# Performance work log

Measured on AMD Instinct MI355X. Metric: run time of the kernel, lower is better.

The kernel has to match this reference:

```python
import jax, jax.numpy as jnp
import numpy as np

N, NC, E, S = 65536, 24576, 524288, 256
VAR_DIM, H1, H2, H3, H4 = 6, 128, 128, 256, 128
THRE, EPS = 0.7, 1e-5


def _bn(x, g, b):
    # BatchNorm1d, training-mode batch statistics (biased var), dropout treated as identity
    mu = x.mean(0)
    v = x.var(0)
    return (x - mu) * jax.lax.rsqrt(v + EPS) * g + b


def _gcn_sparse(h, src, dst, ew, W, b):
    # PyG GCNConv with edge weights: add self-loops (weight 1), symmetric normalization
    n = h.shape[0]
    loop = jnp.arange(n)
    s = jnp.concatenate([src, loop])
    d = jnp.concatenate([dst, loop])
    w = jnp.concatenate([ew, jnp.ones((n,), h.dtype)])
    deg = jax.ops.segment_sum(w, d, num_segments=n)
    dinv = jnp.where(deg > 0, jax.lax.rsqrt(deg), 0.0)
    norm = dinv[s] * w * dinv[d]
    xw = h @ W.T  # [n, out]
    out = jax.ops.segment_sum(norm[:, None] * xw[s], d, num_segments=n)
    return out + b


def _gcn_dense(h, A, W, b):
    # GCNConv on a dense binary adjacency (no edge weights), self-loops + sym norm
    n = h.shape[0]
    A_hat = A + jnp.eye(n, dtype=h.dtype)
    deg = A_hat.sum(0)
    dinv = jnp.where(deg > 0, jax.lax.rsqrt(deg), 0.0)
    return dinv[:, None] * (A_hat.T @ ((h @ W.T) * dinv[:, None])) + b


def setup_inputs() -> dict:
    key = jax.random.key(0)
    ks = jax.random.split(key, 10)

    def w(k, o, i):
        return jax.random.normal(k, (o, i), jnp.float32) / np.float32(np.sqrt(i))

    x = jax.random.normal(ks[0], (N, VAR_DIM), jnp.float32)
    edge_attr = jax.random.uniform(ks[1], (E,), jnp.float32)
    scen_adj = jax.random.uniform(ks[2], (S, S), jnp.float32)
    edge_index = jax.random.randint(ks[3], (2, E), 0, N)
    batch = jnp.arange(N) // (N // S)  # sorted node->graph ids, 256 nodes per graph
    mark = jnp.concatenate([jnp.ones((NC,), jnp.int32), jnp.zeros((N - NC,), jnp.int32)])
    return {
        "x": x, "edge_attr": edge_attr, "scen_adj": scen_adj,
        "mlp_var_w": w(ks[4], H1, VAR_DIM), "mlp_var_b": jnp.zeros((H1,), jnp.float32),
        "mlp_con_w": w(ks[5], H1, 1), "mlp_con_b": jnp.zeros((H1,), jnp.float32),
        "conv1_w": w(ks[6], H2, H1), "conv1_b": jnp.zeros((H2,), jnp.float32),
        "conv2_w": w(ks[7], H3, H2), "conv2_b": jnp.zeros((H3,), jnp.float32),
        "conv3_w": w(ks[8], H4, H3), "conv3_b": jnp.zeros((H4,), jnp.float32),
        "bn1_g": jnp.ones((H1,), jnp.float32), "bn1_b": jnp.zeros((H1,), jnp.float32),
        "bn2_g": jnp.ones((H2,), jnp.float32), "bn2_b": jnp.zeros((H2,), jnp.float32),
        "bn3_g": jnp.ones((H3,), jnp.float32), "bn3_b": jnp.zeros((H3,), jnp.float32),
        "mark": mark, "edge_index": edge_index, "batch": batch, "n_con": NC,
    }


def reference(x, edge_attr, scen_adj, mlp_var_w, mlp_var_b, mlp_con_w, mlp_con_b,
              conv1_w, conv1_b, conv2_w, conv2_b, conv3_w, conv3_b,
              bn1_g, bn1_b, bn2_g, bn2_b, bn3_g, bn3_b,
              mark, edge_index, batch, n_con):
    nc = int(n_con)  # mark layout: first nc nodes are constraints (mark==1), rest vars
    con_feat = jnp.tanh(x[:nc, 0:1] @ mlp_con_w.T + mlp_con_b)
    var_feat = jnp.tanh(x[nc:] @ mlp_var_w.T + mlp_var_b)
    h = jnp.concatenate([con_feat, var_feat], axis=0)  # [N, H1], con-first as in torch cat
    h = _bn(h, bn1_g, bn1_b)  # dropout = identity (eval)
    h = _gcn_sparse(h, edge_index[0], edge_index[1], edge_attr, conv1_w, conv1_b)
    h = jnp.tanh(_bn(h, bn2_g, bn2_b))
    s = scen_adj.shape[0]
    sums = jax.ops.segment_sum(h, batch, num_segments=s)
    cnt = jax.ops.segment_sum(jnp.ones((h.shape[0],), h.dtype), batch, num_segments=s)
    pooled = sums / jnp.maximum(cnt, 1.0)[:, None]  # global_mean_pool -> [S, H2]
    A = (scen_adj >= THRE).astype(h.dtype)  # filter_adj + unweighted edges
    f = jnp.tanh(_bn(_gcn_dense(pooled, A, conv2_w, conv2_b), bn3_g, bn3_b))
    feat = jnp.tanh(_gcn_dense(f, A, conv3_w, conv3_b))
    return feat, feat.mean(0)
```

## Files before the change

kernel.cpp:

```cpp
#include <hip/hip_runtime.h>
#include <hip/hip_bf16.h>
#include <cstddef>

#define N_NODES 65536
#define N_EDGES 524288
#define S_GRAPH 256
#define BN_EPS 1e-5f
#define THRE 0.7f

typedef __hip_bfloat16 bf16;
typedef unsigned int uint32;
typedef unsigned char uchar;
typedef unsigned short ushort16;
typedef __attribute__((ext_vector_type(8))) short short8;
typedef __attribute__((ext_vector_type(4))) float f32x4;

__device__ __forceinline__ float blo(uint32 u) { return __uint_as_float(u << 16); }
__device__ __forceinline__ float bhi(uint32 u) { return __uint_as_float(u & 0xffff0000u); }

__device__ __forceinline__ uint32 packbf(float a, float b)
{
    bf16 ha = __float2bfloat16(a), hb = __float2bfloat16(b);
    unsigned short ua, ub;
    __builtin_memcpy(&ua, &ha, 2); __builtin_memcpy(&ub, &hb, 2);
    return (uint32)ua | ((uint32)ub << 16);
}

__device__ __forceinline__ float ftanh(float x)
{
    float e = __builtin_amdgcn_exp2f(x * 2.8853900817779268f);
    return 1.0f - 2.0f * __builtin_amdgcn_rcpf(e + 1.0f);
}

__global__ __launch_bounds__(256) void k_mlp_hist(
    const float* __restrict__ x, const float* __restrict__ wv,
    const float* __restrict__ bv, const float* __restrict__ wc,
    const float* __restrict__ bc, const int* __restrict__ nconp,
    uint32* __restrict__ h0u, float* __restrict__ pstat,
    const int* __restrict__ dst, uint32* __restrict__ blkhist,
    const float* __restrict__ scen, float* __restrict__ fcol,
    const float* __restrict__ w1f, uint32* __restrict__ w1bk,
    float* __restrict__ zacc, int* __restrict__ ctrs)
{
    __shared__ float xs[128 * 6];
    __shared__ float sh[256];
    __shared__ uint32 bh[256];
    int t = threadIdx.x;
    int b = blockIdx.x;
    if (b < 512) {
        bh[t] = 0;
        __syncthreads();
        int e0 = b * 1024 + t * 4;
        int4 d4 = *(const int4*)(dst + e0);
        atomicAdd(&bh[d4.x >> 8], 1u);
        atomicAdd(&bh[d4.y >> 8], 1u);
        atomicAdd(&bh[d4.z >> 8], 1u);
        atomicAdd(&bh[d4.w >> 8], 1u);
        __syncthreads();
        blkhist[b * 256 + t] = bh[t];
        return;
    }
    if (b >= 1024) {
        if (b == 1024) {
            float s = 0.f;
            for (int r = 0; r < 256; r++)
                s += (scen[r * 256 + t] >= THRE) ? 1.0f : 0.0f;
            fcol[t] = s;
        } else if (b == 1056) {
            const float4* w4 = (const float4*)w1f;
            uint2* wo = (uint2*)w1bk;
            #pragma unroll
            for (int it = 0; it < 16; it++) {
                int fi = it * 256 + t;
                float4 w = w4[fi];
                wo[fi] = make_uint2(packbf(w.x, w.y), packbf(w.z, w.w));
            }
            for (int i = t; i < 7168; i += 256) zacc[i] = 0.f;
            if (t < 8) ctrs[t] = 0;
        }
        return;
    }
    int n0 = (b - 512) * 128;
    if (t < 192) ((float4*)xs)[t] = ((const float4*)(x + (size_t)n0 * 6))[t];
    __syncthreads();

    int nc = *nconp;
    int lane = t & 63, wave = t >> 6;
    int j0 = 2 * lane;
    const float2* wv2 = (const float2*)wv;
    float2 wa0 = wv2[j0 * 3], wa1 = wv2[j0 * 3 + 1], wa2 = wv2[j0 * 3 + 2];
    float2 wb0 = wv2[j0 * 3 + 3], wb1 = wv2[j0 * 3 + 4], wb2 = wv2[j0 * 3 + 5];
    float wc0 = wc[j0], wc1 = wc[j0 + 1], bc0 = bc[j0], bc1 = bc[j0 + 1];
    float bv0 = bv[j0], bv1 = bv[j0 + 1];

    float s0 = 0.f, ss0 = 0.f, s1 = 0.f, ss1 = 0.f;
    #pragma unroll 4
    for (int m = 0; m < 32; m++) {
        int ln = wave * 32 + m;
        int n = n0 + ln;
        const float* xr = &xs[ln * 6];
        float a0, a1;
        if (n < nc) {
            float xv = xr[0];
            a0 = xv * wc0 + bc0; a1 = xv * wc1 + bc1;
        } else {
            float x0 = xr[0], x1 = xr[1], x2 = xr[2], x3 = xr[3], x4 = xr[4], x5 = xr[5];
            a0 = bv0 + x0 * wa0.x + x1 * wa0.y + x2 * wa1.x + x3 * wa1.y + x4 * wa2.x + x5 * wa2.y;
            a1 = bv1 + x0 * wb0.x + x1 * wb0.y + x2 * wb1.x + x3 * wb1.y + x4 * wb2.x + x5 * wb2.y;
        }
        uint32 pk = packbf(ftanh(a0), ftanh(a1));
        h0u[(size_t)n * 64 + lane] = pk;
        float v0 = blo(pk), v1 = bhi(pk);
        s0 += v0; ss0 += v0 * v0; s1 += v1; ss1 += v1 * v1;
    }
    float* pst = pstat + (size_t)(b - 512) * 256;
    sh[t] = s0; __syncthreads();
    if (t < 64) pst[2 * t] = sh[t] + sh[t + 64] + sh[t + 128] + sh[t + 192];
    __syncthreads(); sh[t] = s1; __syncthreads();
    if (t < 64) pst[2 * t + 1] = sh[t] + sh[t + 64] + sh[t + 128] + sh[t + 192];
    __syncthreads(); sh[t] = ss0; __syncthreads();
    if (t < 64) pst[128 + 2 * t] = sh[t] + sh[t + 64] + sh[t + 128] + sh[t + 192];
    __syncthreads(); sh[t] = ss1; __syncthreads();
    if (t < 64) pst[128 + 2 * t + 1] = sh[t] + sh[t + 64] + sh[t + 128] + sh[t + 192];
}

__global__ __launch_bounds__(256) void k_binscan(
    const uint32* __restrict__ blkhist, uint32* __restrict__ blkoff,
    uint32* __restrict__ binsz, uint32* __restrict__ ubase,
    uint32* __restrict__ pbase, const float* __restrict__ pstat,
    float* __restrict__ stats, int* __restrict__ ctr)
{
    __shared__ uint32 v[512];
    __shared__ uint32 ps[256];
    __shared__ int flag;
    int g = blockIdx.x, t = threadIdx.x;
    if (g == 256) {
        float acc = 0.f;
        for (int j = 0; j < 512; j++) acc += pstat[j * 256 + t];
        stats[t] = acc;
        return;
    }
    v[t]       = blkhist[t * 256 + g];
    v[t + 256] = blkhist[(t + 256) * 256 + g];
    __syncthreads();
    uint32 a0 = v[2 * t], a1 = v[2 * t + 1];
    ps[t] = a0 + a1; __syncthreads();
    for (int o = 1; o < 256; o <<= 1) {
        uint32 u = (t >= o) ? ps[t - o] : 0;
        __syncthreads();
        ps[t] += u;
        __syncthreads();
    }
    uint32 ex = ps[t] - (a0 + a1);
    ((uint2*)blkoff)[g * 256 + t] = make_uint2(ex, ex + a0);
    if (t == 255) atomicExch((int*)&binsz[g], (int)ps[255]);
    __syncthreads();
    if (t == 0) {
        __threadfence();
        flag = (atomicAdd(ctr, 1) == 255) ? 1 : 0;
    }
    __syncthreads();
    if (flag) {
        __threadfence();
        uint32 s = binsz[t];
        ps[t] = s; __syncthreads();
        for (int o = 1; o < 256; o <<= 1) {
            uint32 u = (t >= o) ? ps[t - o] : 0;
            __syncthreads();
            ps[t] += u;
            __syncthreads();
        }
        ubase[t] = ps[t] - s;
        pbase[t] = ps[t] - s + (uint32)t * 768u;
    }
}

__global__ __launch_bounds__(256) void k_scatter(
    const int* __restrict__ src, const int* __restrict__ dst,
    const float* __restrict__ ew, const uint32* __restrict__ blkoff,
    const uint32* __restrict__ ubase, uint2* __restrict__ ebin)
{
    __shared__ uint32 bh[256];
    __shared__ uint32 bo[256];
    int b = blockIdx.x, t = threadIdx.x;
    bh[t] = 0;
    bo[t] = ubase[t] + blkoff[t * 512 + b];
    __syncthreads();
    int e0 = b * 1024 + t * 4;
    int4 d4 = *(const int4*)(dst + e0);
    int4 s4 = *(const int4*)(src + e0);
    float4 w4 = *(const float4*)(ew + e0);
    int bin; uint32 r;
    bin = d4.x >> 8; r = atomicAdd(&bh[bin], 1u);
    ebin[bo[bin] + r] = make_uint2((uint32)s4.x | ((uint32)(d4.x & 255) << 16), __float_as_uint(w4.x));
    bin = d4.y >> 8; r = atomicAdd(&bh[bin], 1u);
    ebin[bo[bin] + r] = make_uint2((uint32)s4.y | ((uint32)(d4.y & 255) << 16), __float_as_uint(w4.y));
    bin = d4.z >> 8; r = atomicAdd(&bh[bin], 1u);
    ebin[bo[bin] + r] = make_uint2((uint32)s4.z | ((uint32)(d4.z & 255) << 16), __float_as_uint(w4.z));
    bin = d4.w >> 8; r = atomicAdd(&bh[bin], 1u);
    ebin[bo[bin] + r] = make_uint2((uint32)s4.w | ((uint32)(d4.w & 255) << 16), __float_as_uint(w4.w));
}

__global__ __launch_bounds__(256) void k_csr(
    const uint2* __restrict__ ebin, const uint32* __restrict__ binsz,
    const uint32* __restrict__ ubase, const uint32* __restrict__ pbase,
    float* __restrict__ dinv, int* __restrict__ rowp, int* __restrict__ cnts,
    int2* __restrict__ epk)
{
    __shared__ uint2 es[3072];
    __shared__ uint32 hist[256];
    __shared__ int sscan[256];
    __shared__ int rloc[256];
    __shared__ float dlv[256];
    int g = blockIdx.x, t = threadIdx.x;
    int start = (int)ubase[g];
    int sz = min((int)binsz[g], 3072);
    int pb = (int)pbase[g];
    hist[t] = 0;
    __syncthreads();
    for (int i = t; i < sz; i += 256) {
        uint2 e = ebin[start + i];
        int dl = (e.x >> 16) & 255;
        uint32 wfix = __float2uint_rn(__uint_as_float(e.y) * 262144.0f);
        uint32 h = atomicAdd(&hist[dl], (1u << 24) | wfix);
        e.x |= (h >> 24) << 24;
        es[i] = e;
    }
    __syncthreads();
    uint32 hv = hist[t];
    int cnt = (int)(hv >> 24);
    float di = rsqrtf((float)(hv & 0xFFFFFFu) * 3.814697265625e-6f + 1.0f);
    dlv[t] = di;
    dinv[g * 256 + t] = di;
    cnts[g * 256 + t] = cnt;
    int pcnt = (cnt + 3) & ~3;
    sscan[t] = pcnt; __syncthreads();
    for (int o = 1; o < 256; o <<= 1) {
        int u = (t >= o) ? sscan[t - o] : 0;
        __syncthreads();
        sscan[t] += u;
        __syncthreads();
    }
    int rl = sscan[t] - pcnt;
    rloc[t] = rl;
    rowp[g * 256 + t] = pb + rl;
    __syncthreads();
    for (int i = t; i < sz; i += 256) {
        uint2 e = es[i];
        int s  = (int)(e.x & 0xFFFFu);
        int dl = (int)((e.x >> 16) & 255u);
        int r  = (int)(e.x >> 24);
        float w = __uint_as_float(e.y) * dlv[dl];
        epk[pb + rloc[dl] + r] = make_int2(s, __float_as_int(w));
    }
    int base = pb + rl;
    for (int q = cnt; q < pcnt; q++) epk[base + q] = make_int2(g * 256 + t, 0);
}

__global__ __launch_bounds__(256) void k_gemm1f(
    const uint32* __restrict__ h0u, const uint32* __restrict__ w1bk,
    const float* __restrict__ g1, const float* __restrict__ bb1,
    const float* __restrict__ stats, ushort16* __restrict__ xws,
    const float* __restrict__ dinv)
{
    __shared__ short hn_s[64 * 136];
    __shared__ short w_s[128 * 136];
    __shared__ float sc[128], sf[128];
    int t = threadIdx.x;
    int blk = blockIdx.x;
    int row0 = blk * 64;

    if (t < 128) {
        float mu  = stats[t] * (1.0f / N_NODES);
        float var = stats[128 + t] * (1.0f / N_NODES) - mu * mu;
        float rs  = rsqrtf(fmaxf(var, 0.f) + BN_EPS);
        float s   = rs * g1[t];
        sc[t] = s;
        sf[t] = bb1[t] - mu * s;
    }
    __syncthreads();

    const uint4* h4 = (const uint4*)(h0u + (size_t)row0 * 64);
    #pragma unroll
    for (int it = 0; it < 4; it++) {
        int slot = it * 256 + t;
        int r = slot >> 4, k0 = (slot & 15) * 8;
        uint4 u = h4[slot];
        uint32 ua[4] = {u.x, u.y, u.z, u.w};
        uint32 o[4];
        #pragma unroll
        for (int m = 0; m < 4; m++) {
            int k = k0 + 2 * m;
            o[m] = packbf(blo(ua[m]) * sc[k] + sf[k], bhi(ua[m]) * sc[k + 1] + sf[k + 1]);
        }
        *(uint4*)&hn_s[r * 136 + k0] = make_uint4(o[0], o[1], o[2], o[3]);
    }
    const uint4* wv4 = (const uint4*)w1bk;
    #pragma unroll
    for (int it = 0; it < 8; it++) {
        int s2 = it * 256 + t;
        int c = s2 >> 4, k0 = (s2 & 15) * 8;
        *(uint4*)&w_s[c * 136 + k0] = wv4[s2];
    }
    __syncthreads();

    int lane = t & 63, wave = t >> 6;
    int m16 = lane & 15, kh = lane >> 4;
    int mbase = wave * 16;
    f32x4 acc[8] = {};
    #pragma unroll
    for (int ks = 0; ks < 4; ks++) {
        short8 a = *(const short8*)&hn_s[(mbase + m16) * 136 + ks * 32 + kh * 8];
        #pragma unroll
        for (int ct = 0; ct < 8; ct++) {
            short8 bfr = *(const short8*)&w_s[(ct * 16 + m16) * 136 + ks * 32 + kh * 8];
            acc[ct] = __builtin_amdgcn_mfma_f32_16x16x32_bf16(a, bfr, acc[ct], 0, 0, 0);
        }
    }
    float dvr[4];
    #pragma unroll
    for (int r = 0; r < 4; r++) dvr[r] = dinv[row0 + mbase + kh * 4 + r];
    #pragma unroll
    for (int ct = 0; ct < 8; ct++) {
        int col = ct * 16 + m16;
        #pragma unroll
        for (int r = 0; r < 4; r++) {
            int row = mbase + kh * 4 + r;
            bf16 hv = __float2bfloat16(acc[ct][r] * dvr[r]);
            unsigned short us; __builtin_memcpy(&us, &hv, 2);
            xws[(size_t)(row0 + row) * 128 + col] = us;
        }
    }
}

__global__ __launch_bounds__(256) void k_gather(
    const int* __restrict__ rowp, const int* __restrict__ cnts,
    const int2* __restrict__ epk, const uint32* __restrict__ xwu,
    const float* __restrict__ dinv, const float2* __restrict__ b1c2,
    uint32* __restrict__ aggu, float* __restrict__ stats2r)
{
    __shared__ float sh[256];
    int t = threadIdx.x, b = blockIdx.x;
    int lane = t & 63, wave = t >> 6;
    float2 bb = b1c2[lane];
    float s0 = 0.f, ss0 = 0.f, s1 = 0.f, ss1 = 0.f;
    for (int it = 0; it < 8; it++) {
        int n = b * 32 + it * 4 + wave;
        int st = rowp[n];
        int pcnt = (cnts[n] + 3) & ~3;
        float di = dinv[n];
        uint32 u0 = xwu[(size_t)n * 64 + lane];
        float ax = di * blo(u0) + bb.x;
        float ay = di * bhi(u0) + bb.y;
        int en = st + pcnt;
        int p = st;
        for (; p + 8 <= en; p += 8) {
            int2 q0 = epk[p],     q1 = epk[p + 1], q2 = epk[p + 2], q3 = epk[p + 3];
            int2 q4 = epk[p + 4], q5 = epk[p + 5], q6 = epk[p + 6], q7 = epk[p + 7];
            uint32 v0 = xwu[(size_t)q0.x * 64 + lane];
            uint32 v1 = xwu[(size_t)q1.x * 64 + lane];
            uint32 v2 = xwu[(size_t)q2.x * 64 + lane];
            uint32 v3 = xwu[(size_t)q3.x * 64 + lane];
            uint32 v4 = xwu[(size_t)q4.x * 64 + lane];
            uint32 v5 = xwu[(size_t)q5.x * 64 + lane];
            uint32 v6 = xwu[(size_t)q6.x * 64 + lane];
            uint32 v7 = xwu[(size_t)q7.x * 64 + lane];
            float w0 = __int_as_float(q0.y), w1 = __int_as_float(q1.y);
            float w2 = __int_as_float(q2.y), w3 = __int_as_float(q3.y);
            float w4 = __int_as_float(q4.y), w5 = __int_as_float(q5.y);
            float w6 = __int_as_float(q6.y), w7 = __int_as_float(q7.y);
            ax += w0 * blo(v0) + w1 * blo(v1) + w2 * blo(v2) + w3 * blo(v3);
            ay += w0 * bhi(v0) + w1 * bhi(v1) + w2 * bhi(v2) + w3 * bhi(v3);
            ax += w4 * blo(v4) + w5 * blo(v5) + w6 * blo(v6) + w7 * blo(v7);
            ay += w4 * bhi(v4) + w5 * bhi(v5) + w6 * bhi(v6) + w7 * bhi(v7);
        }
        if (p < en) {
            int2 q0 = epk[p], q1 = epk[p + 1], q2 = epk[p + 2], q3 = epk[p + 3];
            uint32 v0 = xwu[(size_t)q0.x * 64 + lane];
            uint32 v1 = xwu[(size_t)q1.x * 64 + lane];
            uint32 v2 = xwu[(size_t)q2.x * 64 + lane];
            uint32 v3 = xwu[(size_t)q3.x * 64 + lane];
            float w0 = __int_as_float(q0.y), w1 = __int_as_float(q1.y);
            float w2 = __int_as_float(q2.y), w3 = __int_as_float(q3.y);
            ax += w0 * blo(v0) + w1 * blo(v1) + w2 * blo(v2) + w3 * blo(v3);
            ay += w0 * bhi(v0) + w1 * bhi(v1) + w2 * bhi(v2) + w3 * bhi(v3);
        }
        uint32 pk = packbf(ax, ay);
        aggu[(size_t)n * 64 + lane] = pk;
        float v0 = blo(pk), v1 = bhi(pk);
        s0 += v0; ss0 += v0 * v0; s1 += v1; ss1 += v1 * v1;
    }
    float* st2 = stats2r + (b & 7) * 256;
    sh[t] = s0; __syncthreads();
    if (t < 64) atomicAdd(&st2[2 * t], sh[t] + sh[t + 64] + sh[t + 128] + sh[t + 192]);
    __syncthreads(); sh[t] = s1; __syncthreads();
    if (t < 64) atomicAdd(&st2[2 * t + 1], sh[t] + sh[t + 64] + sh[t + 128] + sh[t + 192]);
    __syncthreads(); sh[t] = ss0; __syncthreads();
    if (t < 64) atomicAdd(&st2[128 + 2 * t], sh[t] + sh[t + 64] + sh[t + 128] + sh[t + 192]);
    __syncthreads(); sh[t] = ss1; __syncthreads();
    if (t < 64) atomicAdd(&st2[128 + 2 * t + 1], sh[t] + sh[t + 64] + sh[t + 128] + sh[t + 192]);
}

__global__ __launch_bounds__(512) void k_poolg2(
    const uint32* __restrict__ aggu, const float* __restrict__ stats2r,
    const float* __restrict__ g2, const float* __restrict__ bb2,
    const float* __restrict__ w2, float* __restrict__ z1)
{
    __shared__ float sc[128], sf[128], sh[512], prow[128];
    int t = threadIdx.x, g = blockIdx.x;
    if (t < 128) {
        float su = 0.f, sq = 0.f;
        #pragma unroll
        for (int r = 0; r < 8; r++) {
            su += stats2r[r * 256 + t];
            sq += stats2r[r * 256 + 128 + t];
        }
        float mu  = su * (1.0f / N_NODES);
        float var = sq * (1.0f / N_NODES) - mu * mu;
        float rs  = rsqrtf(fmaxf(var, 0.f) + BN_EPS);
        float s   = rs * g2[t];
        sc[t] = s;
        sf[t] = bb2[t] - mu * s;
    }
    __syncthreads();
    int c = t & 63, grp = t >> 6;
    float c0s = sc[2 * c], c0f = sf[2 * c], c1s = sc[2 * c + 1], c1f = sf[2 * c + 1];
    const uint32* base = aggu + (size_t)g * 256 * 64;
    float s0 = 0.f, s1 = 0.f;
    for (int r = grp * 32; r < grp * 32 + 32; r++) {
        uint32 u = base[r * 64 + c];
        s0 += ftanh(blo(u) * c0s + c0f);
        s1 += ftanh(bhi(u) * c1s + c1f);
    }
    sh[t] = s0; __syncthreads();
    if (t < 64) {
        float acc = 0.f;
        #pragma unroll
        for (int k = 0; k < 8; k++) acc += sh[t + 64 * k];
        prow[2 * t] = acc * (1.0f / 256.0f);
    }
    __syncthreads(); sh[t] = s1; __syncthreads();
    if (t < 64) {
        float acc = 0.f;
        #pragma unroll
        for (int k = 0; k < 8; k++) acc += sh[t + 64 * k];
        prow[2 * t + 1] = acc * (1.0f / 256.0f);
    }
    __syncthreads();
    if (t < 256) {
        float acc = 0.f;
        const float* wr = w2 + t * 128;
        for (int k = 0; k < 128; k++) acc += prow[k] * wr[k];
        z1[g * 256 + t] = acc;
    }
}

__global__ void k_dgcn1(const float* __restrict__ scen, const float* __restrict__ fcol,
                        const float* __restrict__ z1, const float* __restrict__ b2c,
                        float* __restrict__ y1, float* __restrict__ stats3r)
{
    __shared__ float wk[256];
    int i = blockIdx.x, t = threadIdx.x;
    float a = (scen[t * 256 + i] >= THRE) ? 1.0f : 0.0f;
    if (t == i) a += 1.0f;
    wk[t] = a * rsqrtf(fcol[t] + 1.0f);
    __syncthreads();
    float acc = 0.f;
    for (int k = 0; k < 256; k++) acc += wk[k] * z1[k * 256 + t];
    float v = rsqrtf(fcol[i] + 1.0f) * acc + b2c[t];
    y1[i * 256 + t] = v;
    float* s3 = stats3r + (i & 7) * 512;
    atomicAdd(&s3[t], v);
    atomicAdd(&s3[256 + t], v * v);
}

__global__ void k_gemm3(const float* __restrict__ y1, const float* __restrict__ stats3r,
                        const float* __restrict__ g3, const float* __restrict__ bb3,
                        const float* __restrict__ w3, float* __restrict__ z2)
{
    __shared__ float row[256];
    int i = blockIdx.x, t = threadIdx.x;
    for (int c = t; c < 256; c += 128) {
        float s = 0.f, ss = 0.f;
        #pragma unroll
        for (int r = 0; r < 8; r++) {
            s  += stats3r[r * 512 + c];
            ss += stats3r[r * 512 + 256 + c];
        }
        float mu  = s * (1.0f / 256.0f);
        float var = ss * (1.0f / 256.0f) - mu * mu;
        float rs  = rsqrtf(fmaxf(var, 0.f) + BN_EPS);
        float scj = rs * g3[c];
        float sfj = bb3[c] - mu * scj;
        row[c] = ftanh(y1[i * 256 + c] * scj + sfj);
    }
    __syncthreads();
    float acc = 0.f;
    const float* wr = w3 + t * 256;
    for (int k = 0; k < 256; k++) acc += row[k] * wr[k];
    z2[i * 128 + t] = acc;
}

__global__ void k_dgcn2(const float* __restrict__ scen, const float* __restrict__ fcol,
                        const float* __restrict__ z2, const float* __restrict__ b3c,
                        float* __restrict__ out, float* __restrict__ meanr,
                        int* __restrict__ ctr)
{
    __shared__ float wk[256];
    __shared__ int flag;
    int i = blockIdx.x, t = threadIdx.x;
    for (int k = t; k < 256; k += 128) {
        float a = (scen[k * 256 + i] >= THRE) ? 1.0f : 0.0f;
        if (k == i) a += 1.0f;
        wk[k] = a * rsqrtf(fcol[k] + 1.0f);
    }
    __syncthreads();
    float acc = 0.f;
    for (int k = 0; k < 256; k++) acc += wk[k] * z2[k * 128 + t];
    float v = ftanh(rsqrtf(fcol[i] + 1.0f) * acc + b3c[t]);
    out[i * 128 + t] = v;
    atomicAdd(&meanr[(i & 7) * 128 + t], v);
    __syncthreads();
    if (t == 0) {
        __threadfence();
        flag = (atomicAdd(ctr, 1) == 255) ? 1 : 0;
    }
    __syncthreads();
    if (flag) {
        __threadfence();
        float s = 0.f;
        #pragma unroll
        for (int r = 0; r < 8; r++) s += meanr[r * 128 + t];
        out[S_GRAPH * 128 + t] = s * (1.0f / 256.0f);
    }
}

extern "C" void kernel_launch(void* const* d_in, const int* in_sizes, int n_in,
                              void* d_out, int out_size, void* d_ws, size_t ws_size,
                              hipStream_t stream)
{
    const float* x        = (const float*)d_in[0];
    const float* edge_attr= (const float*)d_in[1];
    const float* scen     = (const float*)d_in[2];
    const float* wv       = (const float*)d_in[3];
    const float* bv       = (const float*)d_in[4];
    const float* wc       = (const float*)d_in[5];
    const float* bc       = (const float*)d_in[6];
    const float* w1       = (const float*)d_in[7];
    const float* b1c      = (const float*)d_in[8];
    const float* w2       = (const float*)d_in[9];
    const float* b2c      = (const float*)d_in[10];
    const float* w3       = (const float*)d_in[11];
    const float* b3c      = (const float*)d_in[12];
    const float* g1       = (const float*)d_in[13];
    const float* bb1      = (const float*)d_in[14];
    const float* g2       = (const float*)d_in[15];
    const float* bb2      = (const float*)d_in[16];
    const float* g3       = (const float*)d_in[17];
    const float* bb3      = (const float*)d_in[18];
    const int*  ei        = (const int*)d_in[20];
    const int*  nconp     = (const int*)d_in[22];
    const int*  src = ei;
    const int*  dst = ei + N_EDGES;

    float* wsf = (float*)d_ws;
    uint32*   h0u  = (uint32*)wsf;
    uint32*   aggu = (uint32*)wsf;
    uint32*   xwu  = (uint32*)(wsf + 4194304);
    float* zb      = wsf + 8388608;
    float* stats1  = zb;
    float* zacc    = zb + 512;
    float* stats2r = zacc;
    float* stats3r = zacc + 2048;
    float* meanr   = zacc + 6144;
    float* fcol    = zb + 7680;
    int*   ctrs    = (int*)(zb + 7936);
    float* deg     = zb + 7944;
    int*   rowp    = (int*)(deg + 65536);
    int*   cnts    = rowp + 65536;
    uint32* blkhist= (uint32*)(cnts + 65536);
    uint32* blkoff = blkhist + 131072;
    uint32* binsz  = blkoff + 131072;
    uint32* ubase  = binsz + 256;
    uint32* pbase  = ubase + 256;
    uint2* ebin    = (uint2*)(pbase + 256);
    int2*  epk     = (int2*)(ebin + 524288);
    uint32* w1bk   = (uint32*)(epk + 720896);
    float* z1      = (float*)(w1bk + 8192);
    float* y1      = z1 + 65536;
    float* z2      = y1 + 65536;
    float* pstat   = z2 + 32768;

    float* out = (float*)d_out;

    k_mlp_hist<<<1057, 256, 0, stream>>>(x, wv, bv, wc, bc, nconp, h0u, pstat,
                                         dst, blkhist, scen, fcol, w1, w1bk,
                                         zacc, ctrs);
    k_binscan<<<257, 256, 0, stream>>>(blkhist, blkoff, binsz, ubase, pbase,
                                       pstat, stats1, &ctrs[0]);
    k_scatter<<<512, 256, 0, stream>>>(src, dst, edge_attr, blkoff, ubase, ebin);
    k_csr<<<256, 256, 0, stream>>>(ebin, binsz, ubase, pbase, deg, rowp, cnts, epk);
    k_gemm1f<<<1024, 256, 0, stream>>>(h0u, w1bk, g1, bb1, stats1, (ushort16*)xwu, deg);
    k_gather<<<2048, 256, 0, stream>>>(rowp, cnts, epk, xwu, deg,
                                       (const float2*)b1c, aggu, stats2r);
    k_poolg2<<<S_GRAPH, 512, 0, stream>>>(aggu, stats2r, g2, bb2, w2, z1);
    k_dgcn1<<<256, 256, 0, stream>>>(scen, fcol, z1, b2c, y1, stats3r);
    k_gemm3<<<256, 128, 0, stream>>>(y1, stats3r, g3, bb3, w3, z2);
    k_dgcn2<<<256, 128, 0, stream>>>(scen, fcol, z2, b3c, out, meanr, &ctrs[1]);
}
```

Before: 238.8 us.

## Fuse edge scatter with GEMM1 and move dinv row scaling into CSR kernel

The edge scatter and the BN+GEMM1 kernel are merged into a single 1536-block launch. Blocks below 512 bin edges and the rest compute the normalized-feature GEMM, so the two independent stages overlap and one launch is removed. The GEMM no longer depends on dinv, so the per-row dinv scaling now happens at the end of k_csr, which reads and rewrites each bin's 256 xw rows in place. The cost is an extra read-modify-write pass over xw (16 MB bf16), a second bf16 rounding of xw, and a shared-memory footprint sized for the GEMM that also applies to the scatter blocks.

```diff
diff --git a/kernel.cpp b/kernel.cpp
--- a/kernel.cpp
+++ b/kernel.cpp
@@ -175,37 +175,108 @@
     }
 }
 
-__global__ __launch_bounds__(256) void k_scatter(
+__global__ __launch_bounds__(256) void k_sg(
     const int* __restrict__ src, const int* __restrict__ dst,
     const float* __restrict__ ew, const uint32* __restrict__ blkoff,
-    const uint32* __restrict__ ubase, uint2* __restrict__ ebin)
-{
-    __shared__ uint32 bh[256];
-    __shared__ uint32 bo[256];
-    int b = blockIdx.x, t = threadIdx.x;
-    bh[t] = 0;
-    bo[t] = ubase[t] + blkoff[t * 512 + b];
-    __syncthreads();
-    int e0 = b * 1024 + t * 4;
-    int4 d4 = *(const int4*)(dst + e0);
-    int4 s4 = *(const int4*)(src + e0);
-    float4 w4 = *(const float4*)(ew + e0);
-    int bin; uint32 r;
-    bin = d4.x >> 8; r = atomicAdd(&bh[bin], 1u);
-    ebin[bo[bin] + r] = make_uint2((uint32)s4.x | ((uint32)(d4.x & 255) << 16), __float_as_uint(w4.x));
-    bin = d4.y >> 8; r = atomicAdd(&bh[bin], 1u);
-    ebin[bo[bin] + r] = make_uint2((uint32)s4.y | ((uint32)(d4.y & 255) << 16), __float_as_uint(w4.y));
-    bin = d4.z >> 8; r = atomicAdd(&bh[bin], 1u);
-    ebin[bo[bin] + r] = make_uint2((uint32)s4.z | ((uint32)(d4.z & 255) << 16), __float_as_uint(w4.z));
-    bin = d4.w >> 8; r = atomicAdd(&bh[bin], 1u);
-    ebin[bo[bin] + r] = make_uint2((uint32)s4.w | ((uint32)(d4.w & 255) << 16), __float_as_uint(w4.w));
+    const uint32* __restrict__ ubase, uint2* __restrict__ ebin,
+    const uint32* __restrict__ h0u, const uint32* __restrict__ w1bk,
+    const float* __restrict__ g1, const float* __restrict__ bb1,
+    const float* __restrict__ stats, ushort16* __restrict__ xws)
+{
+    __shared__ __align__(16) uchar smem[53248];
+    int t = threadIdx.x, b = blockIdx.x;
+    if (b < 512) {
+        uint32* bh = (uint32*)smem;
+        uint32* bo = (uint32*)(smem + 1024);
+        bh[t] = 0;
+        bo[t] = ubase[t] + blkoff[t * 512 + b];
+        __syncthreads();
+        int e0 = b * 1024 + t * 4;
+        int4 d4 = *(const int4*)(dst + e0);
+        int4 s4 = *(const int4*)(src + e0);
+        float4 w4 = *(const float4*)(ew + e0);
+        int bin; uint32 r;
+        bin = d4.x >> 8; r = atomicAdd(&bh[bin], 1u);
+        ebin[bo[bin] + r] = make_uint2((uint32)s4.x | ((uint32)(d4.x & 255) << 16), __float_as_uint(w4.x));
+        bin = d4.y >> 8; r = atomicAdd(&bh[bin], 1u);
+        ebin[bo[bin] + r] = make_uint2((uint32)s4.y | ((uint32)(d4.y & 255) << 16), __float_as_uint(w4.y));
+        bin = d4.z >> 8; r = atomicAdd(&bh[bin], 1u);
+        ebin[bo[bin] + r] = make_uint2((uint32)s4.z | ((uint32)(d4.z & 255) << 16), __float_as_uint(w4.z));
+        bin = d4.w >> 8; r = atomicAdd(&bh[bin], 1u);
+        ebin[bo[bin] + r] = make_uint2((uint32)s4.w | ((uint32)(d4.w & 255) << 16), __float_as_uint(w4.w));
+        return;
+    }
+    short* hn_s = (short*)smem;
+    short* w_s  = (short*)(smem + 17408);
+    float* sc   = (float*)(smem + 52224);
+    float* sf   = (float*)(smem + 52736);
+    int row0 = (b - 512) * 64;
+
+    if (t < 128) {
+        float mu  = stats[t] * (1.0f / N_NODES);
+        float var = stats[128 + t] * (1.0f / N_NODES) - mu * mu;
+        float rs  = rsqrtf(fmaxf(var, 0.f) + BN_EPS);
+        float s   = rs * g1[t];
+        sc[t] = s;
+        sf[t] = bb1[t] - mu * s;
+    }
+    __syncthreads();
+
+    const uint4* h4 = (const uint4*)(h0u + (size_t)row0 * 64);
+    #pragma unroll
+    for (int it = 0; it < 4; it++) {
+        int slot = it * 256 + t;
+        int r = slot >> 4, k0 = (slot & 15) * 8;
+        uint4 u = h4[slot];
+        uint32 ua[4] = {u.x, u.y, u.z, u.w};
+        uint32 o[4];
+        #pragma unroll
+        for (int m = 0; m < 4; m++) {
+            int k = k0 + 2 * m;
+            o[m] = packbf(blo(ua[m]) * sc[k] + sf[k], bhi(ua[m]) * sc[k + 1] + sf[k + 1]);
+        }
+        *(uint4*)&hn_s[r * 136 + k0] = make_uint4(o[0], o[1], o[2], o[3]);
+    }
+    const uint4* wv4 = (const uint4*)w1bk;
+    #pragma unroll
+    for (int it = 0; it < 8; it++) {
+        int s2 = it * 256 + t;
+        int c = s2 >> 4, k0 = (s2 & 15) * 8;
+        *(uint4*)&w_s[c * 136 + k0] = wv4[s2];
+    }
+    __syncthreads();
+
+    int lane = t & 63, wave = t >> 6;
+    int m16 = lane & 15, kh = lane >> 4;
+    int mbase = wave * 16;
+    f32x4 acc[8] = {};
+    #pragma unroll
+    for (int ks = 0; ks < 4; ks++) {
+        short8 a = *(const short8*)&hn_s[(mbase + m16) * 136 + ks * 32 + kh * 8];
+        #pragma unroll
+        for (int ct = 0; ct < 8; ct++) {
+            short8 bfr = *(const short8*)&w_s[(ct * 16 + m16) * 136 + ks * 32 + kh * 8];
+            acc[ct] = __builtin_amdgcn_mfma_f32_16x16x32_bf16(a, bfr, acc[ct], 0, 0, 0);
+        }
+    }
+    #pragma unroll
+    for (int ct = 0; ct < 8; ct++) {
+        int col = ct * 16 + m16;
+        #pragma unroll
+        for (int r = 0; r < 4; r++) {
+            int row = mbase + kh * 4 + r;
+            bf16 hv = __float2bfloat16(acc[ct][r]);
+            unsigned short us; __builtin_memcpy(&us, &hv, 2);
+            xws[(size_t)(row0 + row) * 128 + col] = us;
+        }
+    }
 }
 
 __global__ __launch_bounds__(256) void k_csr(
     const uint2* __restrict__ ebin, const uint32* __restrict__ binsz,
     const uint32* __restrict__ ubase, const uint32* __restrict__ pbase,
     float* __restrict__ dinv, int* __restrict__ rowp, int* __restrict__ cnts,
-    int2* __restrict__ epk)
+    int2* __restrict__ epk, uint32* __restrict__ xwu)
 {
     __shared__ uint2 es[3072];
     __shared__ uint32 hist[256];
@@ -255,81 +326,15 @@
     }
     int base = pb + rl;
     for (int q = cnt; q < pcnt; q++) epk[base + q] = make_int2(g * 256 + t, 0);
-}
-
-__global__ __launch_bounds__(256) void k_gemm1f(
-    const uint32* __restrict__ h0u, const uint32* __restrict__ w1bk,
-    const float* __restrict__ g1, const float* __restrict__ bb1,
-    const float* __restrict__ stats, ushort16* __restrict__ xws,
-    const float* __restrict__ dinv)
-{
-    __shared__ short hn_s[64 * 136];
-    __shared__ short w_s[128 * 136];
-    __shared__ float sc[128], sf[128];
-    int t = threadIdx.x;
-    int blk = blockIdx.x;
-    int row0 = blk * 64;
-
-    if (t < 128) {
-        float mu  = stats[t] * (1.0f / N_NODES);
-        float var = stats[128 + t] * (1.0f / N_NODES) - mu * mu;
-        float rs  = rsqrtf(fmaxf(var, 0.f) + BN_EPS);
-        float s   = rs * g1[t];
-        sc[t] = s;
-        sf[t] = bb1[t] - mu * s;
-    }
-    __syncthreads();
-
-    const uint4* h4 = (const uint4*)(h0u + (size_t)row0 * 64);
-    #pragma unroll
-    for (int it = 0; it < 4; it++) {
-        int slot = it * 256 + t;
-        int r = slot >> 4, k0 = (slot & 15) * 8;
-        uint4 u = h4[slot];
-        uint32 ua[4] = {u.x, u.y, u.z, u.w};
-        uint32 o[4];
-        #pragma unroll
-        for (int m = 0; m < 4; m++) {
-            int k = k0 + 2 * m;
-            o[m] = packbf(blo(ua[m]) * sc[k] + sf[k], bhi(ua[m]) * sc[k + 1] + sf[k + 1]);
-        }
-        *(uint4*)&hn_s[r * 136 + k0] = make_uint4(o[0], o[1], o[2], o[3]);
-    }
-    const uint4* wv4 = (const uint4*)w1bk;
-    #pragma unroll
-    for (int it = 0; it < 8; it++) {
-        int s2 = it * 256 + t;
-        int c = s2 >> 4, k0 = (s2 & 15) * 8;
-        *(uint4*)&w_s[c * 136 + k0] = wv4[s2];
-    }
-    __syncthreads();
-
-    int lane = t & 63, wave = t >> 6;
-    int m16 = lane & 15, kh = lane >> 4;
-    int mbase = wave * 16;
-    f32x4 acc[8] = {};
-    #pragma unroll
-    for (int ks = 0; ks < 4; ks++) {
-        short8 a = *(const short8*)&hn_s[(mbase + m16) * 136 + ks * 32 + kh * 8];
-        #pragma unroll
-        for (int ct = 0; ct < 8; ct++) {
-            short8 bfr = *(const short8*)&w_s[(ct * 16 + m16) * 136 + ks * 32 + kh * 8];
-            acc[ct] = __builtin_amdgcn_mfma_f32_16x16x32_bf16(a, bfr, acc[ct], 0, 0, 0);
-        }
-    }
-    float dvr[4];
-    #pragma unroll
-    for (int r = 0; r < 4; r++) dvr[r] = dinv[row0 + mbase + kh * 4 + r];
-    #pragma unroll
-    for (int ct = 0; ct < 8; ct++) {
-        int col = ct * 16 + m16;
-        #pragma unroll
-        for (int r = 0; r < 4; r++) {
-            int row = mbase + kh * 4 + r;
-            bf16 hv = __float2bfloat16(acc[ct][r] * dvr[r]);
-            unsigned short us; __builtin_memcpy(&us, &hv, 2);
-            xws[(size_t)(row0 + row) * 128 + col] = us;
-        }
+    uint4* xr = (uint4*)(xwu + (size_t)g * 256 * 64);
+    for (int i = t; i < 4096; i += 256) {
+        float d = dlv[i >> 4];
+        uint4 u = xr[i];
+        u.x = packbf(blo(u.x) * d, bhi(u.x) * d);
+        u.y = packbf(blo(u.y) * d, bhi(u.y) * d);
+        u.z = packbf(blo(u.z) * d, bhi(u.z) * d);
+        u.w = packbf(blo(u.w) * d, bhi(u.w) * d);
+        xr[i] = u;
     }
 }
 
@@ -598,9 +603,10 @@
                                          zacc, ctrs);
     k_binscan<<<257, 256, 0, stream>>>(blkhist, blkoff, binsz, ubase, pbase,
                                        pstat, stats1, &ctrs[0]);
-    k_scatter<<<512, 256, 0, stream>>>(src, dst, edge_attr, blkoff, ubase, ebin);
-    k_csr<<<256, 256, 0, stream>>>(ebin, binsz, ubase, pbase, deg, rowp, cnts, epk);
-    k_gemm1f<<<1024, 256, 0, stream>>>(h0u, w1bk, g1, bb1, stats1, (ushort16*)xwu, deg);
+    k_sg<<<1536, 256, 0, stream>>>(src, dst, edge_attr, blkoff, ubase, ebin,
+                                   h0u, w1bk, g1, bb1, stats1, (ushort16*)xwu);
+    k_csr<<<256, 256, 0, stream>>>(ebin, binsz, ubase, pbase, deg, rowp, cnts,
+                                   epk, xwu);
     k_gather<<<2048, 256, 0, stream>>>(rowp, cnts, epk, xwu, deg,
                                        (const float2*)b1c, aggu, stats2r);
     k_poolg2<<<S_GRAPH, 512, 0, stream>>>(aggu, stats2r, g2, bb2, w2, z1);
```

Result: no change. 237.9 us (-0.4%).
